# Kernel tuning notes

Measured on AMD Instinct MI355X. Metric: run time of the kernel, lower is better.

## Reference

```python
import jax, jax.numpy as jnp
import numpy as np

N, E = 10000, 160000
IN_C, HID, K = 128, 256, 16


def setup_inputs() -> dict:
    key = jax.random.key(0)
    ks = jax.random.split(key, 8)
    x = jax.random.normal(ks[0], (N, IN_C), jnp.float32)
    edge_index = jax.random.randint(ks[1], (2, E), 0, N, dtype=jnp.int32).astype(jnp.int64)
    edge_attributes = jax.random.uniform(ks[2], (E,), jnp.float32)
    W1 = jax.random.normal(ks[3], (IN_C, HID), jnp.float32) / np.sqrt(IN_C)
    b1 = jnp.zeros((HID,), jnp.float32)
    W2 = jax.random.normal(ks[4], (HID, HID), jnp.float32) / np.sqrt(HID)
    b2 = jnp.zeros((HID,), jnp.float32)
    Wp = jax.random.normal(ks[5], (HID, K), jnp.float32) / np.sqrt(HID)
    bp = jnp.zeros((K,), jnp.float32)
    return dict(x=x, edge_index=edge_index, edge_attributes=edge_attributes,
                W1=W1, b1=b1, W2=W2, b2=b2, Wp=Wp, bp=bp)


def _gcn_conv(x, src, dst, ew, W, b):
    """GCNConv with add_self_loops=True, normalize=True, edge weights."""
    n = x.shape[0]
    loop = jnp.arange(n)
    s = jnp.concatenate([src, loop])
    d = jnp.concatenate([dst, loop])
    w = jnp.concatenate([ew, jnp.ones((n,), x.dtype)])
    deg = jax.ops.segment_sum(w, d, num_segments=n)           # weighted in-degree
    dis = jnp.where(deg > 0, jax.lax.rsqrt(deg), 0.0)         # D^{-1/2}, inf -> 0
    norm = dis[s] * w * dis[d]                                # per-edge coefficient
    h = x @ W                                                 # transform first
    msg = norm[:, None] * h[s]                                # gather from source
    out = jax.ops.segment_sum(msg, d, num_segments=n)         # scatter-add to target
    return out + b


def reference(x, edge_index, edge_attributes, W1, b1, W2, b2, Wp, bp):
    src, dst = edge_index[0], edge_index[1]
    ew = edge_attributes
    h = jax.nn.relu(_gcn_conv(x, src, dst, ew, W1, b1))
    h = jax.nn.relu(_gcn_conv(h, src, dst, ew, W2, b2))

    # to_dense_adj (duplicate edges accumulate)
    adj = jnp.zeros((N, N), h.dtype).at[src, dst].add(ew)

    # DMoNPooling (dropout=0, eval): s = softmax(Linear(h))
    s = jax.nn.softmax(h @ Wp + bp, axis=-1)                  # [N, K]

    out_adj = s.T @ adj @ s                                   # [K, K]
    deg = adj.sum(axis=1)                                     # [N]
    m = deg.sum() / 2
    ca = s.T @ deg[:, None]                                   # [K, 1]
    cb = deg[None, :] @ s                                     # [1, K]
    normalizer = (ca @ cb) / (2 * m)
    spectral_loss = -jnp.trace(out_adj - normalizer) / (2 * m)

    cluster_size = s.sum(axis=0)                              # [K]
    cluster_loss = jnp.linalg.norm(cluster_size) / N * jnp.sqrt(jnp.float32(K)) - 1.0

    loss = 100.0 * (spectral_loss + cluster_loss)
    # PyG returns s with a leading batch dim of 1
    return s[None], loss, 100.0 * spectral_loss, 100.0 * cluster_loss
```

## Files before the change

kernel.cpp:

```cpp
#include <hip/hip_runtime.h>
#include <math.h>


#define ER_BLOCKS 128

typedef unsigned short u16;
typedef __attribute__((ext_vector_type(8))) short short8v;
typedef __attribute__((ext_vector_type(4))) float float4v;
typedef __attribute__((ext_vector_type(4))) unsigned short ushort4v;

__device__ __forceinline__ u16 f2bf_rne(float x) {
  unsigned u = __float_as_uint(x);
  u = (u + 0x7fffu + ((u >> 16) & 1u)) >> 16;
  return (u16)u;
}
__device__ __forceinline__ float bf2f(u16 h) {
  return __uint_as_float(((unsigned)h) << 16);
}

__device__ __forceinline__ bool ei_is_i64(const int* __restrict__ ei) {
  return ((ei[1] | ei[3] | ei[5] | ei[7]) == 0);
}
__device__ __forceinline__ int ld_idx(const int* __restrict__ ei, int pos, bool i64) {
  return i64 ? ei[2 * pos] : ei[pos];
}

__global__ __launch_bounds__(256) void zero_init(int4* __restrict__ p, int n4) {
  int i = blockIdx.x * 256 + threadIdx.x;
  if (i < n4) p[i] = make_int4(0, 0, 0, 0);
}

__global__ __launch_bounds__(256) void conv_weights(const float* __restrict__ W1,
                                                    const float* __restrict__ W2,
                                                    u16* __restrict__ w1hi, u16* __restrict__ w1lo,
                                                    u16* __restrict__ w2hi, u16* __restrict__ w2lo) {
  const int T1 = 256 * 128;
  const int T2 = 256 * 256;
  int t = blockIdx.x * 256 + threadIdx.x;
  if (t < T1) {
    int n = t >> 7, k = t & 127;
    float x = W1[k * 256 + n];
    u16 h = f2bf_rne(x);
    w1hi[t] = h;
    w1lo[t] = f2bf_rne(x - bf2f(h));
  } else if (t < T1 + T2) {
    int t2 = t - T1;
    int n = t2 >> 8, k = t2 & 255;
    float x = W2[k * 256 + n];
    u16 h = f2bf_rne(x);
    w2hi[t2] = h;
    w2lo[t2] = f2bf_rne(x - bf2f(h));
  }
}

__global__ __launch_bounds__(256) void edge_count(const int* __restrict__ ei,
                                                  const float* __restrict__ ew,
                                                  int* __restrict__ cnt,
                                                  float* __restrict__ deg, int E) {
  int e = blockIdx.x * 256 + threadIdx.x;
  if (e >= E) return;
  bool i64 = ei_is_i64(ei);
  int d = ld_idx(ei, E + e, i64);
  atomicAdd(&cnt[d], 1);
  atomicAdd(&deg[d], ew[e]);
}

__global__ __launch_bounds__(1024) void scan_kernel(const int* __restrict__ cnt,
                                                    int* __restrict__ rowptr, int n) {
  __shared__ int sums[1024];
  int tid = threadIdx.x;
  int CH = (n + 1023) >> 10;
  int beg = tid * CH, end = min(beg + CH, n);
  int s = 0;
  for (int i = beg; i < end; ++i) s += cnt[i];
  sums[tid] = s;
  __syncthreads();
  for (int off = 1; off < 1024; off <<= 1) {
    int v = (tid >= off) ? sums[tid - off] : 0;
    __syncthreads();
    sums[tid] += v;
    __syncthreads();
  }
  int run = (tid == 0) ? 0 : sums[tid - 1];
  for (int i = beg; i < end; ++i) { rowptr[i] = run; run += cnt[i]; }
  if (tid == 1023) rowptr[n] = run;
}

__global__ __launch_bounds__(256) void scatter_edges(const int* __restrict__ ei,
                                                     const float* __restrict__ ew,
                                                     const int* __restrict__ rowptr,
                                                     int* __restrict__ cur,
                                                     const float* __restrict__ deg,
                                                     int* __restrict__ col,
                                                     float* __restrict__ coef, int E) {
  int e = blockIdx.x * 256 + threadIdx.x;
  if (e >= E) return;
  bool i64 = ei_is_i64(ei);
  int s = ld_idx(ei, e, i64);
  int d = ld_idx(ei, E + e, i64);
  int p = rowptr[d] + atomicAdd(&cur[d], 1);
  col[p] = s;
  float ds = 1.0f / sqrtf(deg[s] + 1.0f);
  float dd = 1.0f / sqrtf(deg[d] + 1.0f);
  coef[p] = ds * ew[e] * dd;
}

template <int CH>
__global__ __launch_bounds__(256) void aggregate_pre(const float* __restrict__ src,
                                                     const int* __restrict__ rowptr,
                                                     const int* __restrict__ col,
                                                     const float* __restrict__ coef,
                                                     const float* __restrict__ deg,
                                                     u16* __restrict__ ohi,
                                                     u16* __restrict__ olo, int N) {
  constexpr int Q = CH / 4;
  constexpr int NS = 256 / Q;
  int i = blockIdx.x;
  int t = threadIdx.x;
  int q = t % Q, slot = t / Q;
  int e0 = rowptr[i], e1 = rowptr[i + 1];
  float4 acc = make_float4(0.f, 0.f, 0.f, 0.f);
  for (int p = e0 + slot; p < e1; p += NS) {
    int c = col[p];
    float w = coef[p];
    float4 v = *reinterpret_cast<const float4*>(&src[(size_t)c * CH + q * 4]);
    acc.x += w * v.x; acc.y += w * v.y; acc.z += w * v.z; acc.w += w * v.w;
  }
  __shared__ float4 red[256];
  red[t] = acc;
  __syncthreads();
  if (slot == 0) {
#pragma unroll
    for (int s2 = 1; s2 < NS; ++s2) {
      float4 o = red[s2 * Q + q];
      acc.x += o.x; acc.y += o.y; acc.z += o.z; acc.w += o.w;
    }
    float w0 = 1.0f / (deg[i] + 1.0f);
    float4 xv = *reinterpret_cast<const float4*>(&src[(size_t)i * CH + q * 4]);
    acc.x += w0 * xv.x; acc.y += w0 * xv.y; acc.z += w0 * xv.z; acc.w += w0 * xv.w;
    float a[4] = {acc.x, acc.y, acc.z, acc.w};
    ushort4v hv, lv;
#pragma unroll
    for (int j = 0; j < 4; ++j) {
      u16 h = f2bf_rne(a[j]);
      hv[j] = h;
      lv[j] = f2bf_rne(a[j] - bf2f(h));
    }
    *reinterpret_cast<ushort4v*>(&ohi[(size_t)i * CH + q * 4]) = hv;
    *reinterpret_cast<ushort4v*>(&olo[(size_t)i * CH + q * 4]) = lv;
  }
}

__global__ __launch_bounds__(256) void gemm_mfma(const u16* __restrict__ Ahi,
                                                 const u16* __restrict__ Alo,
                                                 const u16* __restrict__ Wthi,
                                                 const u16* __restrict__ Wtlo,
                                                 const float* __restrict__ bias,
                                                 float* __restrict__ C,
                                                 int M, int K) {
  __shared__ u16 As_hi[64][40], As_lo[64][40];
  __shared__ u16 Bs_hi[64][40], Bs_lo[64][40];
  int tid = threadIdx.x;
  int w = tid >> 6, l = tid & 63;
  int wm = w >> 1, wn = w & 1;
  int row0 = blockIdx.x * 64, col0 = blockIdx.y * 64;
  int srow = tid >> 2, sc = (tid & 3) * 8;
  int fr = l & 15, kg = (l >> 4) * 8;

  float4v acc[2][2];
#pragma unroll
  for (int i = 0; i < 2; ++i)
#pragma unroll
    for (int j = 0; j < 2; ++j) acc[i][j] = (float4v){0.f, 0.f, 0.f, 0.f};

  for (int k0 = 0; k0 < K; k0 += 32) {
    {
      int gr = row0 + srow;
      uint4 zero = make_uint4(0, 0, 0, 0);
      uint4 vh = zero, vl = zero;
      if (gr < M) {
        vh = *reinterpret_cast<const uint4*>(&Ahi[(size_t)gr * K + k0 + sc]);
        vl = *reinterpret_cast<const uint4*>(&Alo[(size_t)gr * K + k0 + sc]);
      }
      *reinterpret_cast<uint4*>(&As_hi[srow][sc]) = vh;
      *reinterpret_cast<uint4*>(&As_lo[srow][sc]) = vl;
      int bn = col0 + srow;
      uint4 bh = *reinterpret_cast<const uint4*>(&Wthi[(size_t)bn * K + k0 + sc]);
      uint4 bl = *reinterpret_cast<const uint4*>(&Wtlo[(size_t)bn * K + k0 + sc]);
      *reinterpret_cast<uint4*>(&Bs_hi[srow][sc]) = bh;
      *reinterpret_cast<uint4*>(&Bs_lo[srow][sc]) = bl;
    }
    __syncthreads();
    short8v ah[2], al[2], bh[2], bl[2];
#pragma unroll
    for (int i = 0; i < 2; ++i) {
      int r = wm * 32 + i * 16 + fr;
      ah[i] = *reinterpret_cast<const short8v*>(&As_hi[r][kg]);
      al[i] = *reinterpret_cast<const short8v*>(&As_lo[r][kg]);
    }
#pragma unroll
    for (int j = 0; j < 2; ++j) {
      int n = wn * 32 + j * 16 + fr;
      bh[j] = *reinterpret_cast<const short8v*>(&Bs_hi[n][kg]);
      bl[j] = *reinterpret_cast<const short8v*>(&Bs_lo[n][kg]);
    }
#pragma unroll
    for (int i = 0; i < 2; ++i)
#pragma unroll
      for (int j = 0; j < 2; ++j) {
        acc[i][j] = __builtin_amdgcn_mfma_f32_16x16x32_bf16(ah[i], bh[j], acc[i][j], 0, 0, 0);
        acc[i][j] = __builtin_amdgcn_mfma_f32_16x16x32_bf16(al[i], bh[j], acc[i][j], 0, 0, 0);
        acc[i][j] = __builtin_amdgcn_mfma_f32_16x16x32_bf16(ah[i], bl[j], acc[i][j], 0, 0, 0);
      }
    __syncthreads();
  }
#pragma unroll
  for (int j = 0; j < 2; ++j) {
    int gc = col0 + wn * 32 + j * 16 + fr;
    float bj = bias[gc];
#pragma unroll
    for (int i = 0; i < 2; ++i) {
#pragma unroll
      for (int r = 0; r < 4; ++r) {
        int gr = row0 + wm * 32 + i * 16 + (l >> 4) * 4 + r;
        if (gr < M) {
          float v = acc[i][j][r] + bj;
          C[(size_t)gr * 256 + gc] = fmaxf(v, 0.0f);
        }
      }
    }
  }
}

__global__ __launch_bounds__(256) void pool_kernel(const float* __restrict__ h,
                                                   const float* __restrict__ Wp,
                                                   const float* __restrict__ bp,
                                                   float* __restrict__ s_out,
                                                   float* __restrict__ cs_part, int N) {
  __shared__ float Wps[256 * 16];
  __shared__ float cs_loc[16];
  int tid = threadIdx.x;
  for (int idx = tid; idx < 4096; idx += 256) Wps[idx] = Wp[idx];
  if (tid < 16) cs_loc[tid] = 0.f;
  __syncthreads();
  int lane = tid & 63;
  int wave = tid >> 6;
  int k = lane & 15, g = lane >> 4;
  int node = blockIdx.x * 16 + wave * 4 + g;
  float acc = 0.f;
  if (node < N) {
    const float4* hrow = reinterpret_cast<const float4*>(h + (size_t)node * 256);
#pragma unroll 8
    for (int c4 = 0; c4 < 64; ++c4) {
      float4 hv = hrow[c4];
      int cb = c4 * 4;
      acc += hv.x * Wps[(cb + 0) * 16 + k];
      acc += hv.y * Wps[(cb + 1) * 16 + k];
      acc += hv.z * Wps[(cb + 2) * 16 + k];
      acc += hv.w * Wps[(cb + 3) * 16 + k];
    }
    acc += bp[k];
  }
  float mx = acc;
#pragma unroll
  for (int off = 1; off < 16; off <<= 1) mx = fmaxf(mx, __shfl_xor(mx, off));
  float ex = (node < N) ? expf(acc - mx) : 0.f;
  float sm = ex;
#pragma unroll
  for (int off = 1; off < 16; off <<= 1) sm += __shfl_xor(sm, off);
  float sval = (node < N) ? ex / sm : 0.f;
  if (node < N) s_out[(size_t)node * 16 + k] = sval;
  float v = sval;
  v += __shfl_xor(v, 16);
  v += __shfl_xor(v, 32);
  if (lane < 16) atomicAdd(&cs_loc[lane], v);
  __syncthreads();
  if (tid < 16) cs_part[(size_t)blockIdx.x * 16 + tid] = cs_loc[tid];
}

__global__ __launch_bounds__(256) void edge_reduce(const int* __restrict__ ei,
                                                   const float* __restrict__ ew,
                                                   const float* __restrict__ s,
                                                   float* __restrict__ part, int E) {
  __shared__ float loc[18];
  int tid = threadIdx.x;
  if (tid < 18) loc[tid] = 0.f;
  __syncthreads();
  bool i64 = ei_is_i64(ei);
  float dot = 0.f, w = 0.f;
  float ca[16];
#pragma unroll
  for (int k = 0; k < 16; ++k) ca[k] = 0.f;
  for (int e = blockIdx.x * 256 + tid; e < E; e += gridDim.x * 256) {
    int a = ld_idx(ei, e, i64);
    int b = ld_idx(ei, E + e, i64);
    float we = ew[e];
    const float4* sa = reinterpret_cast<const float4*>(s + (size_t)a * 16);
    const float4* sb = reinterpret_cast<const float4*>(s + (size_t)b * 16);
    float d = 0.f;
#pragma unroll
    for (int q = 0; q < 4; ++q) {
      float4 av = sa[q], bv = sb[q];
      d += av.x * bv.x + av.y * bv.y + av.z * bv.z + av.w * bv.w;
      ca[q * 4 + 0] += we * av.x; ca[q * 4 + 1] += we * av.y;
      ca[q * 4 + 2] += we * av.z; ca[q * 4 + 3] += we * av.w;
    }
    dot += we * d;
    w += we;
  }
#pragma unroll
  for (int off = 32; off; off >>= 1) {
    dot += __shfl_xor(dot, off);
    w += __shfl_xor(w, off);
#pragma unroll
    for (int k = 0; k < 16; ++k) ca[k] += __shfl_xor(ca[k], off);
  }
  if ((tid & 63) == 0) {
    atomicAdd(&loc[0], dot);
    atomicAdd(&loc[1], w);
#pragma unroll
    for (int k = 0; k < 16; ++k) atomicAdd(&loc[2 + k], ca[k]);
  }
  __syncthreads();
  if (tid < 18) part[(size_t)blockIdx.x * 18 + tid] = loc[tid];
}

__global__ __launch_bounds__(256) void finalize(const float* __restrict__ epart,
                                                const float* __restrict__ cs_part,
                                                int pool_blocks,
                                                float* __restrict__ out,
                                                int N, int s_elems) {
  __shared__ float red[18];
  __shared__ float csl[256];
  __shared__ float cs[16];
  int tid = threadIdx.x;
  if (tid < 18) {
    float a = 0.f;
    for (int b = 0; b < ER_BLOCKS; ++b) a += epart[(size_t)b * 18 + tid];
    red[tid] = a;
  }
  {
    int k = tid & 15, sl = tid >> 4;
    float a = 0.f;
    for (int b = sl; b < pool_blocks; b += 16) a += cs_part[(size_t)b * 16 + k];
    csl[tid] = a;
  }
  __syncthreads();
  if (tid < 16) {
    float a = 0.f;
#pragma unroll
    for (int sl = 0; sl < 16; ++sl) a += csl[sl * 16 + tid];
    cs[tid] = a;
  }
  __syncthreads();
  if (tid == 0) {
    float tr = red[0], m2 = red[1];
    float ca2 = 0.f, cs2 = 0.f;
    for (int k = 0; k < 16; ++k) {
      ca2 += red[2 + k] * red[2 + k];
      cs2 += cs[k] * cs[k];
    }
    float sp = -(tr - ca2 / m2) / m2;
    float cl = sqrtf(cs2) / (float)N * 4.0f - 1.0f;
    out[s_elems + 0] = 100.f * (sp + cl);
    out[s_elems + 1] = 100.f * sp;
    out[s_elems + 2] = 100.f * cl;
  }
}

extern "C" void kernel_launch(void* const* d_in, const int* in_sizes, int n_in,
                              void* d_out, int out_size, void* d_ws, size_t ws_size,
                              hipStream_t stream) {
  const float* x  = (const float*)d_in[0];
  const int*   ei = (const int*)d_in[1];
  const float* ew = (const float*)d_in[2];
  const float* W1 = (const float*)d_in[3];
  const float* b1 = (const float*)d_in[4];
  const float* W2 = (const float*)d_in[5];
  const float* b2 = (const float*)d_in[6];
  const float* Wp = (const float*)d_in[7];
  const float* bp = (const float*)d_in[8];
  float* out = (float*)d_out;

  const int IN_C = 128, HID = 256;
  const int N = in_sizes[0] / IN_C;
  const int E = in_sizes[2];
  const int pool_blocks = (N + 15) / 16;

  char* p = (char*)d_ws;
  auto alloc = [&](size_t b) { char* r = p; p += (b + 255) & ~(size_t)255; return r; };
  float* deg     = (float*)alloc((size_t)N * 4);
  int*   cnt     = (int*)alloc((size_t)N * 4);
  int*   cur     = (int*)alloc((size_t)N * 4);
  char*  zero_end = p;
  u16*   axhi    = (u16*)alloc((size_t)N * IN_C * 2);
  u16*   axlo    = (u16*)alloc((size_t)N * IN_C * 2);
  u16*   ahhi    = (u16*)alloc((size_t)N * HID * 2);
  u16*   ahlo    = (u16*)alloc((size_t)N * HID * 2);
  float* h       = (float*)alloc((size_t)N * HID * 4);
  float* h2      = (float*)alloc((size_t)N * HID * 4);
  u16*   w1hi    = (u16*)alloc((size_t)256 * 128 * 2);
  u16*   w1lo    = (u16*)alloc((size_t)256 * 128 * 2);
  u16*   w2hi    = (u16*)alloc((size_t)256 * 256 * 2);
  u16*   w2lo    = (u16*)alloc((size_t)256 * 256 * 2);
  int*   rowptr  = (int*)alloc((size_t)(N + 1) * 4);
  int*   col     = (int*)alloc((size_t)E * 4);
  float* coef    = (float*)alloc((size_t)E * 4);
  float* epart   = (float*)alloc((size_t)ER_BLOCKS * 18 * 4);
  float* cs_part = (float*)alloc((size_t)pool_blocks * 16 * 4);
  if ((size_t)(p - (char*)d_ws) > ws_size) return;

  int zn4 = (int)((zero_end - (char*)deg) >> 4);
  zero_init<<<(zn4 + 255) / 256, 256, 0, stream>>>((int4*)deg, zn4);
  conv_weights<<<(256 * 128 + 256 * 256 + 255) / 256, 256, 0, stream>>>(
      W1, W2, w1hi, w1lo, w2hi, w2lo);

  int eb = (E + 255) / 256;
  edge_count<<<eb, 256, 0, stream>>>(ei, ew, cnt, deg, E);
  scan_kernel<<<1, 1024, 0, stream>>>(cnt, rowptr, N);
  scatter_edges<<<eb, 256, 0, stream>>>(ei, ew, rowptr, cur, deg, col, coef, E);

  dim3 gg((N + 63) / 64, HID / 64);
  aggregate_pre<128><<<N, 256, 0, stream>>>(x, rowptr, col, coef, deg, axhi, axlo, N);
  gemm_mfma<<<gg, 256, 0, stream>>>(axhi, axlo, w1hi, w1lo, b1, h, N, IN_C);
  aggregate_pre<256><<<N, 256, 0, stream>>>(h, rowptr, col, coef, deg, ahhi, ahlo, N);
  gemm_mfma<<<gg, 256, 0, stream>>>(ahhi, ahlo, w2hi, w2lo, b2, h2, N, HID);

  pool_kernel<<<pool_blocks, 256, 0, stream>>>(h2, Wp, bp, out, cs_part, N);
  edge_reduce<<<ER_BLOCKS, 256, 0, stream>>>(ei, ew, out, epart, E);
  finalize<<<1, 256, 0, stream>>>(epart, cs_part, pool_blocks, out, N, N * 16);
}
```

Baseline: 153.7 us.

## Gather bf16 node features in aggregation, fuse setup and finalize kernels

The input features and the first-layer output are stored as single bf16 instead of fp32, which halves the bytes gathered per edge in both aggregation passes. Zero-init, the x conversion and the weight split are merged into one setup kernel. The finalize kernel is folded into edge_reduce through a last-block atomic counter, removing two launches in total. The cost is lower accuracy, because gathered features lose the lo-part precision before the GEMM's hi/lo split.

```diff
diff --git a/kernel.cpp b/kernel.cpp
--- a/kernel.cpp
+++ b/kernel.cpp
@@ -25,31 +25,42 @@
   return i64 ? ei[2 * pos] : ei[pos];
 }
 
-__global__ __launch_bounds__(256) void zero_init(int4* __restrict__ p, int n4) {
-  int i = blockIdx.x * 256 + threadIdx.x;
-  if (i < n4) p[i] = make_int4(0, 0, 0, 0);
-}
-
-__global__ __launch_bounds__(256) void conv_weights(const float* __restrict__ W1,
+__global__ __launch_bounds__(256) void setup_kernel(int4* __restrict__ zp, int zn4,
+                                                    const float* __restrict__ x,
+                                                    u16* __restrict__ xbf, int nx4,
+                                                    const float* __restrict__ W1,
+                                                    u16* __restrict__ w1hi, u16* __restrict__ w1lo,
                                                     const float* __restrict__ W2,
-                                                    u16* __restrict__ w1hi, u16* __restrict__ w1lo,
                                                     u16* __restrict__ w2hi, u16* __restrict__ w2lo) {
-  const int T1 = 256 * 128;
-  const int T2 = 256 * 256;
-  int t = blockIdx.x * 256 + threadIdx.x;
-  if (t < T1) {
-    int n = t >> 7, k = t & 127;
-    float x = W1[k * 256 + n];
-    u16 h = f2bf_rne(x);
-    w1hi[t] = h;
-    w1lo[t] = f2bf_rne(x - bf2f(h));
-  } else if (t < T1 + T2) {
-    int t2 = t - T1;
-    int n = t2 >> 8, k = t2 & 255;
-    float x = W2[k * 256 + n];
-    u16 h = f2bf_rne(x);
-    w2hi[t2] = h;
-    w2lo[t2] = f2bf_rne(x - bf2f(h));
+  const int T1 = 256 * 128, T2 = 256 * 256;
+  int idx = blockIdx.x * 256 + threadIdx.x;
+  if (idx < zn4) {
+    zp[idx] = make_int4(0, 0, 0, 0);
+    return;
+  }
+  idx -= zn4;
+  if (idx < nx4) {
+    float4 v = reinterpret_cast<const float4*>(x)[idx];
+    ushort4v o = {f2bf_rne(v.x), f2bf_rne(v.y), f2bf_rne(v.z), f2bf_rne(v.w)};
+    reinterpret_cast<ushort4v*>(xbf)[idx] = o;
+    return;
+  }
+  idx -= nx4;
+  if (idx < T1) {
+    int n = idx >> 7, k = idx & 127;
+    float v = W1[k * 256 + n];
+    u16 h = f2bf_rne(v);
+    w1hi[idx] = h;
+    w1lo[idx] = f2bf_rne(v - bf2f(h));
+    return;
+  }
+  idx -= T1;
+  if (idx < T2) {
+    int n = idx >> 8, k = idx & 255;
+    float v = W2[k * 256 + n];
+    u16 h = f2bf_rne(v);
+    w2hi[idx] = h;
+    w2lo[idx] = f2bf_rne(v - bf2f(h));
   }
 }
 
@@ -106,7 +117,7 @@
 }
 
 template <int CH>
-__global__ __launch_bounds__(256) void aggregate_pre(const float* __restrict__ src,
+__global__ __launch_bounds__(256) void aggregate_pre(const u16* __restrict__ src,
                                                      const int* __restrict__ rowptr,
                                                      const int* __restrict__ col,
                                                      const float* __restrict__ coef,
@@ -123,8 +134,9 @@
   for (int p = e0 + slot; p < e1; p += NS) {
     int c = col[p];
     float w = coef[p];
-    float4 v = *reinterpret_cast<const float4*>(&src[(size_t)c * CH + q * 4]);
-    acc.x += w * v.x; acc.y += w * v.y; acc.z += w * v.z; acc.w += w * v.w;
+    ushort4v v = *reinterpret_cast<const ushort4v*>(&src[(size_t)c * CH + q * 4]);
+    acc.x += w * bf2f(v[0]); acc.y += w * bf2f(v[1]);
+    acc.z += w * bf2f(v[2]); acc.w += w * bf2f(v[3]);
   }
   __shared__ float4 red[256];
   red[t] = acc;
@@ -136,8 +148,9 @@
       acc.x += o.x; acc.y += o.y; acc.z += o.z; acc.w += o.w;
     }
     float w0 = 1.0f / (deg[i] + 1.0f);
-    float4 xv = *reinterpret_cast<const float4*>(&src[(size_t)i * CH + q * 4]);
-    acc.x += w0 * xv.x; acc.y += w0 * xv.y; acc.z += w0 * xv.z; acc.w += w0 * xv.w;
+    ushort4v xv = *reinterpret_cast<const ushort4v*>(&src[(size_t)i * CH + q * 4]);
+    acc.x += w0 * bf2f(xv[0]); acc.y += w0 * bf2f(xv[1]);
+    acc.z += w0 * bf2f(xv[2]); acc.w += w0 * bf2f(xv[3]);
     float a[4] = {acc.x, acc.y, acc.z, acc.w};
     ushort4v hv, lv;
 #pragma unroll
@@ -157,7 +170,8 @@
                                                  const u16* __restrict__ Wtlo,
                                                  const float* __restrict__ bias,
                                                  float* __restrict__ C,
-                                                 int M, int K) {
+                                                 u16* __restrict__ Cbf,
+                                                 int M, int K, int outbf) {
   __shared__ u16 As_hi[64][40], As_lo[64][40];
   __shared__ u16 Bs_hi[64][40], Bs_lo[64][40];
   int tid = threadIdx.x;
@@ -224,8 +238,9 @@
       for (int r = 0; r < 4; ++r) {
         int gr = row0 + wm * 32 + i * 16 + (l >> 4) * 4 + r;
         if (gr < M) {
-          float v = acc[i][j][r] + bj;
-          C[(size_t)gr * 256 + gc] = fmaxf(v, 0.0f);
+          float v = fmaxf(acc[i][j][r] + bj, 0.0f);
+          if (outbf) Cbf[(size_t)gr * 256 + gc] = f2bf_rne(v);
+          else       C[(size_t)gr * 256 + gc] = v;
         }
       }
     }
@@ -281,7 +296,12 @@
 __global__ __launch_bounds__(256) void edge_reduce(const int* __restrict__ ei,
                                                    const float* __restrict__ ew,
                                                    const float* __restrict__ s,
-                                                   float* __restrict__ part, int E) {
+                                                   float* __restrict__ part,
+                                                   const float* __restrict__ cs_part,
+                                                   int pool_blocks,
+                                                   int* __restrict__ ctr,
+                                                   float* __restrict__ out,
+                                                   int N, int s_elems, int E) {
   __shared__ float loc[18];
   int tid = threadIdx.x;
   if (tid < 18) loc[tid] = 0.f;
@@ -323,20 +343,19 @@
   }
   __syncthreads();
   if (tid < 18) part[(size_t)blockIdx.x * 18 + tid] = loc[tid];
-}
-
-__global__ __launch_bounds__(256) void finalize(const float* __restrict__ epart,
-                                                const float* __restrict__ cs_part,
-                                                int pool_blocks,
-                                                float* __restrict__ out,
-                                                int N, int s_elems) {
+
+  __shared__ bool amLast;
+  __threadfence();
+  if (tid == 0) amLast = (atomicAdd(ctr, 1) == (int)gridDim.x - 1);
+  __syncthreads();
+  if (!amLast) return;
+
   __shared__ float red[18];
   __shared__ float csl[256];
   __shared__ float cs[16];
-  int tid = threadIdx.x;
   if (tid < 18) {
     float a = 0.f;
-    for (int b = 0; b < ER_BLOCKS; ++b) a += epart[(size_t)b * 18 + tid];
+    for (int b = 0; b < (int)gridDim.x; ++b) a += part[(size_t)b * 18 + tid];
     red[tid] = a;
   }
   {
@@ -392,12 +411,14 @@
   float* deg     = (float*)alloc((size_t)N * 4);
   int*   cnt     = (int*)alloc((size_t)N * 4);
   int*   cur     = (int*)alloc((size_t)N * 4);
+  int*   ctr     = (int*)alloc(256);
   char*  zero_end = p;
+  u16*   xbf     = (u16*)alloc((size_t)N * IN_C * 2);
+  u16*   hbf     = (u16*)alloc((size_t)N * HID * 2);
   u16*   axhi    = (u16*)alloc((size_t)N * IN_C * 2);
   u16*   axlo    = (u16*)alloc((size_t)N * IN_C * 2);
   u16*   ahhi    = (u16*)alloc((size_t)N * HID * 2);
   u16*   ahlo    = (u16*)alloc((size_t)N * HID * 2);
-  float* h       = (float*)alloc((size_t)N * HID * 4);
   float* h2      = (float*)alloc((size_t)N * HID * 4);
   u16*   w1hi    = (u16*)alloc((size_t)256 * 128 * 2);
   u16*   w1lo    = (u16*)alloc((size_t)256 * 128 * 2);
@@ -411,9 +432,10 @@
   if ((size_t)(p - (char*)d_ws) > ws_size) return;
 
   int zn4 = (int)((zero_end - (char*)deg) >> 4);
-  zero_init<<<(zn4 + 255) / 256, 256, 0, stream>>>((int4*)deg, zn4);
-  conv_weights<<<(256 * 128 + 256 * 256 + 255) / 256, 256, 0, stream>>>(
-      W1, W2, w1hi, w1lo, w2hi, w2lo);
+  int nx4 = (N * IN_C) / 4;
+  int setup_items = zn4 + nx4 + 256 * 128 + 256 * 256;
+  setup_kernel<<<(setup_items + 255) / 256, 256, 0, stream>>>(
+      (int4*)deg, zn4, x, xbf, nx4, W1, w1hi, w1lo, W2, w2hi, w2lo);
 
   int eb = (E + 255) / 256;
   edge_count<<<eb, 256, 0, stream>>>(ei, ew, cnt, deg, E);
@@ -421,12 +443,12 @@
   scatter_edges<<<eb, 256, 0, stream>>>(ei, ew, rowptr, cur, deg, col, coef, E);
 
   dim3 gg((N + 63) / 64, HID / 64);
-  aggregate_pre<128><<<N, 256, 0, stream>>>(x, rowptr, col, coef, deg, axhi, axlo, N);
-  gemm_mfma<<<gg, 256, 0, stream>>>(axhi, axlo, w1hi, w1lo, b1, h, N, IN_C);
-  aggregate_pre<256><<<N, 256, 0, stream>>>(h, rowptr, col, coef, deg, ahhi, ahlo, N);
-  gemm_mfma<<<gg, 256, 0, stream>>>(ahhi, ahlo, w2hi, w2lo, b2, h2, N, HID);
+  aggregate_pre<128><<<N, 256, 0, stream>>>(xbf, rowptr, col, coef, deg, axhi, axlo, N);
+  gemm_mfma<<<gg, 256, 0, stream>>>(axhi, axlo, w1hi, w1lo, b1, nullptr, hbf, N, IN_C, 1);
+  aggregate_pre<256><<<N, 256, 0, stream>>>(hbf, rowptr, col, coef, deg, ahhi, ahlo, N);
+  gemm_mfma<<<gg, 256, 0, stream>>>(ahhi, ahlo, w2hi, w2lo, b2, h2, nullptr, N, HID, 0);
 
   pool_kernel<<<pool_blocks, 256, 0, stream>>>(h2, Wp, bp, out, cs_part, N);
-  edge_reduce<<<ER_BLOCKS, 256, 0, stream>>>(ei, ew, out, epart, E);
-  finalize<<<1, 256, 0, stream>>>(epart, cs_part, pool_blocks, out, N, N * 16);
-}
+  edge_reduce<<<ER_BLOCKS, 256, 0, stream>>>(ei, ew, out, epart, cs_part, pool_blocks,
+                                             ctr, out, N, N * 16, E);
+}
```

New measurement: 174.3 us. 1.13x slower.
